# Kernel optimization log

Measured on AMD Instinct MI355X. Metric: run time of the kernel, lower is better.

Reference implementation:

```python
import jax, jax.numpy as jnp
import numpy as np

NUM_CLASSES = 80
FOCAL_ALPHA = 0.25
FOCAL_GAMMA = 2.0
HUBER_SIGMA = 3.0
REG_MEAN = 0.0
REG_STD = 0.2
IMG_H = 800.0
IMG_W = 800.0
B, A, M = 4, 100000, 32


def setup_inputs() -> dict:
    key = jax.random.key(0)
    k1, k2, k3, k4, k5, k6, k7 = jax.random.split(key, 7)
    classification = jax.random.uniform(k1, (B, A, NUM_CLASSES), dtype=jnp.float32)
    regression = jax.random.normal(k2, (B, A, 4), dtype=jnp.float32)
    # plausible anchors: centers inside image, sizes 16..256
    cx = jax.random.uniform(k3, (A,), minval=0.0, maxval=IMG_W)
    cy = jax.random.uniform(k4, (A,), minval=0.0, maxval=IMG_H)
    s = jax.random.uniform(k5, (A, 2), minval=16.0, maxval=256.0)
    anchors = jnp.stack([cx - s[:, 0] / 2, cy - s[:, 1] / 2,
                         cx + s[:, 0] / 2, cy + s[:, 1] / 2], axis=1).astype(jnp.float32)
    # annotations: [B, M, 5] = x1,y1,x2,y2,class
    xy = jax.random.uniform(k6, (B, M, 2), minval=0.0, maxval=650.0)
    wh = jax.random.uniform(k7, (B, M, 2), minval=30.0, maxval=150.0)
    cls = jax.random.randint(jax.random.fold_in(key, 9), (B, M, 1), 0, NUM_CLASSES).astype(jnp.float32)
    annotations = jnp.concatenate([xy, xy + wh, cls], axis=-1)
    return {"classification": classification, "regression": regression,
            "anchors": anchors, "annotations": annotations}


def _pairwise_iou(anchors, boxes):
    # anchors [A,4], boxes [M,4] -> [A,M]
    ix1 = jnp.maximum(anchors[:, None, 0], boxes[None, :, 0])
    iy1 = jnp.maximum(anchors[:, None, 1], boxes[None, :, 1])
    ix2 = jnp.minimum(anchors[:, None, 2], boxes[None, :, 2])
    iy2 = jnp.minimum(anchors[:, None, 3], boxes[None, :, 3])
    inter = jnp.clip(ix2 - ix1, 0.0) * jnp.clip(iy2 - iy1, 0.0)
    area_a = (anchors[:, 2] - anchors[:, 0]) * (anchors[:, 3] - anchors[:, 1])
    area_b = (boxes[:, 2] - boxes[:, 0]) * (boxes[:, 3] - boxes[:, 1])
    union = area_a[:, None] + area_b[None, :] - inter
    return inter / jnp.maximum(union, 1e-8)


def _targets(anchors, annotations):
    # per-image anchor assignment, vmapped over batch
    def per_image(ann):
        boxes = ann[:, :4]
        cls = ann[:, 4].astype(jnp.int32)
        ious = _pairwise_iou(anchors, boxes)          # [A,M]
        best = jnp.argmax(ious, axis=1)               # [A]
        best_iou = jnp.max(ious, axis=1)
        pos = best_iou >= 0.5
        ign = (best_iou > 0.4) & (~pos)
        states = jnp.where(pos, 1.0, jnp.where(ign, -1.0, 0.0))
        cx = (anchors[:, 0] + anchors[:, 2]) * 0.5
        cy = (anchors[:, 1] + anchors[:, 3]) * 0.5
        inside = (cx >= 0) & (cx < IMG_W) & (cy >= 0) & (cy < IMG_H)
        states = jnp.where(inside, states, -1.0)
        labels = jax.nn.one_hot(cls[best], NUM_CLASSES, dtype=jnp.float32) * pos[:, None]
        ab = boxes[best]                              # assigned gt boxes [A,4]
        aw = anchors[:, 2] - anchors[:, 0]
        ah = anchors[:, 3] - anchors[:, 1]
        t = jnp.stack([(ab[:, 0] - anchors[:, 0]) / aw,
                       (ab[:, 1] - anchors[:, 1]) / ah,
                       (ab[:, 2] - anchors[:, 2]) / aw,
                       (ab[:, 3] - anchors[:, 3]) / ah], axis=1)
        t = (t - REG_MEAN) / REG_STD
        return labels, t, states
    return jax.vmap(per_image)(annotations)


def reference(classification, regression, anchors, annotations):
    labels, reg_t, states = _targets(anchors, annotations)   # [B,A,K],[B,A,4],[B,A]
    num_pos = jnp.maximum(jnp.sum((states == 1.0).astype(jnp.float32)), 1.0)
    # focal loss over non-ignored anchors
    valid = (states != -1.0)[..., None].astype(jnp.float32)
    p = jnp.clip(classification, 1e-4, 1.0 - 1e-4)
    bce = -(labels * jnp.log(p) + (1.0 - labels) * jnp.log1p(-p))
    alpha_f = jnp.where(labels == 1.0, FOCAL_ALPHA, 1.0 - FOCAL_ALPHA)
    focal_w = alpha_f * jnp.where(labels == 1.0, 1.0 - p, p) ** FOCAL_GAMMA
    cls_loss = jnp.sum(focal_w * bce * valid) / num_pos
    # smooth L1 over positive anchors
    pos_m = (states == 1.0)[..., None].astype(jnp.float32)
    s2 = HUBER_SIGMA ** 2
    d = jnp.abs(regression - reg_t)
    l1 = jnp.where(d < 1.0 / s2, 0.5 * s2 * d * d, d - 0.5 / s2)
    reg_loss = jnp.sum(l1 * pos_m) / num_pos
    return cls_loss + reg_loss
```

## Files before the change

### kernel.cpp

```cpp
#include <hip/hip_runtime.h>

#define BB 4
#define AA 100000
#define MM 32
#define NC 80
#define GX 391
#define NBLK (GX * BB)


__device__ __forceinline__ void gld_lds16(const float4* g, float4* l) {
    __builtin_amdgcn_global_load_lds(
        (const __attribute__((address_space(1))) void*)g,
        (__attribute__((address_space(3))) void*)l,
        16, 0, 0);
}

#define FOCAL_K(vk, flatk)                                                  \
  {                                                                         \
    const int s    = (flatk) / 20;                                          \
    const int colb = ((flatk) - s * 20) * 4;                                \
    const int c    = scode[s];                                              \
    const float m  = (c != -2) ? 1.0f : 0.0f;                               \
    const float q0 = fminf(fmaxf((vk).x, 1e-4f), 0.9999f);                  \
    const float q1 = fminf(fmaxf((vk).y, 1e-4f), 0.9999f);                  \
    const float q2 = fminf(fmaxf((vk).z, 1e-4f), 0.9999f);                  \
    const float q3 = fminf(fmaxf((vk).w, 1e-4f), 0.9999f);                  \
    float sub = 0.0f;                                                       \
    sub += 0.75f * q0 * q0 * (-__logf(1.0f - q0));                          \
    sub += 0.75f * q1 * q1 * (-__logf(1.0f - q1));                          \
    sub += 0.75f * q2 * q2 * (-__logf(1.0f - q2));                          \
    sub += 0.75f * q3 * q3 * (-__logf(1.0f - q3));                          \
    csum += m * sub;                                                        \
    const unsigned rel = (unsigned)(c - colb);                              \
    if (rel < 4u) {      \
      const float p = (rel & 2u) ? ((rel & 1u) ? q3 : q2)                   \
                                 : ((rel & 1u) ? q1 : q0);                  \
      const float onem = 1.0f - p;                                          \
      csum += 0.25f * onem * onem * (-__logf(p))                            \
            - 0.75f * p * p * (-__logf(onem));                              \
    }                                                                       \
  }

#define FOCAL_BATCH(vv, batch)                                              \
  _Pragma("unroll")                                                         \
  for (int k = 0; k < 5; ++k) {                                             \
    const int flat = ((batch) * 5 + k) * 256 + tid;                         \
    FOCAL_K((vv)[k], flat)                                                  \
  }

__global__ __launch_bounds__(256) void fused_kernel(
    const float* __restrict__ anchors,
    const float* __restrict__ annotations,
    const float* __restrict__ regression,
    const float* __restrict__ cls,
    float* __restrict__ cls_part,
    float* __restrict__ reg_part,
    unsigned* __restrict__ pos_part)
{
    __shared__ float ann[MM * 5];
    __shared__ float areab[MM];
    __shared__ int scode[256];
    __shared__ float4 pre[5 * 256];
    const int b = blockIdx.y;
    const int tid = threadIdx.x;
    if (tid < MM * 5) ann[tid] = annotations[b * MM * 5 + tid];
    if (tid < MM) {
        const float bx1 = annotations[b * MM * 5 + tid * 5 + 0];
        const float by1 = annotations[b * MM * 5 + tid * 5 + 1];
        const float bx2 = annotations[b * MM * 5 + tid * 5 + 2];
        const float by2 = annotations[b * MM * 5 + tid * 5 + 3];
        areab[tid] = __fmul_rn(__fsub_rn(bx2, bx1), __fsub_rn(by2, by1));
    }
    __syncthreads();

    const int abase = blockIdx.x * 256;
    const int a = abase + tid;
    const float4* base4 = (const float4*)cls + ((size_t)b * AA + abase) * 20;
    const int maxflat = (abase + 256 <= AA) ? (5120 - 1) : ((AA - abase) * 20 - 1);

    float4 an = make_float4(0.f, 0.f, 0.f, 0.f);
    if (a < AA) an = ((const float4*)anchors)[a];

    #pragma unroll
    for (int k = 0; k < 5; ++k)
        gld_lds16(&base4[min(k * 256 + tid, maxflat)], &pre[k * 256 + tid]);

    float reg_sum = 0.0f;
    int pos_cnt = 0;
    int code = -2;

    if (a < AA) {
        const float ax1 = an.x, ay1 = an.y, ax2 = an.z, ay2 = an.w;
        const float area_a = __fmul_rn(__fsub_rn(ax2, ax1), __fsub_rn(ay2, ay1));

        float best_iou = -1.0f;
        int best = 0;
        #pragma unroll
        for (int j = 0; j < MM; ++j) {
            const float bx1 = ann[j * 5 + 0];
            const float by1 = ann[j * 5 + 1];
            const float bx2 = ann[j * 5 + 2];
            const float by2 = ann[j * 5 + 3];
            const float ix1 = fmaxf(ax1, bx1);
            const float iy1 = fmaxf(ay1, by1);
            const float ix2 = fminf(ax2, bx2);
            const float iy2 = fminf(ay2, by2);
            const float iw = fmaxf(__fsub_rn(ix2, ix1), 0.0f);
            const float ih = fmaxf(__fsub_rn(iy2, iy1), 0.0f);
            const float inter = __fmul_rn(iw, ih);
            const float uni = __fsub_rn(__fadd_rn(area_a, areab[j]), inter);
            const float iou = __fdiv_rn(inter, fmaxf(uni, 1e-8f));
            if (iou > best_iou) { best_iou = iou; best = j; }
        }

        const bool pos = best_iou >= 0.5f;
        const bool ign = (best_iou > 0.4f) && !pos;
        const float cx = (ax1 + ax2) * 0.5f;
        const float cy = (ay1 + ay2) * 0.5f;
        const bool inside = (cx >= 0.0f) && (cx < 800.0f) && (cy >= 0.0f) && (cy < 800.0f);

        const bool valid = inside && !ign;
        if (valid) code = pos ? (int)ann[best * 5 + 4] : -1;

        if (pos && inside) {
            pos_cnt = 1;
            const float aw = ax2 - ax1;
            const float ah = ay2 - ay1;
            const float bx1 = ann[best * 5 + 0];
            const float by1 = ann[best * 5 + 1];
            const float bx2 = ann[best * 5 + 2];
            const float by2 = ann[best * 5 + 3];
            float t[4];
            t[0] = ((bx1 - ax1) / aw) / 0.2f;
            t[1] = ((by1 - ay1) / ah) / 0.2f;
            t[2] = ((bx2 - ax2) / aw) / 0.2f;
            t[3] = ((by2 - ay2) / ah) / 0.2f;
            const float* rg = regression + (((size_t)b * AA + a) * 4);
            #pragma unroll
            for (int k = 0; k < 4; ++k) {
                const float d = fabsf(rg[k] - t[k]);
                reg_sum += (d < (1.0f / 9.0f)) ? (4.5f * d * d) : (d - (0.5f / 9.0f));
            }
        }
    }
    scode[tid] = code;
    __syncthreads();

    float csum = 0.0f;

    float4 v1[5];
    #pragma unroll
    for (int k = 0; k < 5; ++k) v1[k] = base4[min((5 + k) * 256 + tid, maxflat)];

    float4 v0[5];
    #pragma unroll
    for (int k = 0; k < 5; ++k) v0[k] = pre[k * 256 + tid];
    FOCAL_BATCH(v0, 0)

    float4 v2[5];
    #pragma unroll
    for (int k = 0; k < 5; ++k) v2[k] = base4[min((10 + k) * 256 + tid, maxflat)];
    FOCAL_BATCH(v1, 1)

    float4 v3[5];
    #pragma unroll
    for (int k = 0; k < 5; ++k) v3[k] = base4[min((15 + k) * 256 + tid, maxflat)];
    FOCAL_BATCH(v2, 2)
    FOCAL_BATCH(v3, 3)

    #pragma unroll
    for (int off = 32; off > 0; off >>= 1) {
        csum    += __shfl_down(csum, off);
        reg_sum += __shfl_down(reg_sum, off);
        pos_cnt += __shfl_down(pos_cnt, off);
    }
    __shared__ float wc[4], wr[4];
    __shared__ int   wp[4];
    const int wave = tid >> 6, lane = tid & 63;
    if (lane == 0) { wc[wave] = csum; wr[wave] = reg_sum; wp[wave] = pos_cnt; }
    __syncthreads();
    if (tid == 0) {
        const int idx = b * GX + blockIdx.x;
        cls_part[idx] = wc[0] + wc[1] + wc[2] + wc[3];
        reg_part[idx] = wr[0] + wr[1] + wr[2] + wr[3];
        pos_part[idx] = (unsigned)(wp[0] + wp[1] + wp[2] + wp[3]);
    }
}

__global__ __launch_bounds__(256) void finalize_kernel(
    const float* __restrict__ cls_part,
    const float* __restrict__ reg_part,
    const unsigned* __restrict__ pos_part,
    float* __restrict__ out)
{
    float cs = 0.0f, rs = 0.0f;
    unsigned pc = 0;
    for (int i = threadIdx.x; i < NBLK; i += 256) {
        cs += cls_part[i];
        rs += reg_part[i];
        pc += pos_part[i];
    }
    #pragma unroll
    for (int off = 32; off > 0; off >>= 1) {
        cs += __shfl_down(cs, off);
        rs += __shfl_down(rs, off);
        pc += __shfl_down(pc, off);
    }
    __shared__ float wc[4], wr[4];
    __shared__ unsigned wp[4];
    const int wave = threadIdx.x >> 6, lane = threadIdx.x & 63;
    if (lane == 0) { wc[wave] = cs; wr[wave] = rs; wp[wave] = pc; }
    __syncthreads();
    if (threadIdx.x == 0) {
        const float csum = wc[0] + wc[1] + wc[2] + wc[3];
        const float rsum = wr[0] + wr[1] + wr[2] + wr[3];
        const float np = fmaxf((float)(wp[0] + wp[1] + wp[2] + wp[3]), 1.0f);
        out[0] = (csum + rsum) / np;
    }
}

extern "C" void kernel_launch(void* const* d_in, const int* in_sizes, int n_in,
                              void* d_out, int out_size, void* d_ws, size_t ws_size,
                              hipStream_t stream)
{
    const float* classification = (const float*)d_in[0];
    const float* regression     = (const float*)d_in[1];
    const float* anchors        = (const float*)d_in[2];
    const float* annotations    = (const float*)d_in[3];
    float* out = (float*)d_out;

    float*    cls_part = (float*)d_ws;
    float*    reg_part = cls_part + NBLK;
    unsigned* pos_part = (unsigned*)(reg_part + NBLK);

    dim3 grid(GX, BB);
    fused_kernel<<<grid, 256, 0, stream>>>(anchors, annotations, regression,
                                           classification, cls_part, reg_part, pos_part);
    finalize_kernel<<<1, 256, 0, stream>>>(cls_part, reg_part, pos_part, out);
}
```

Baseline: 196.8 us.

## Fuse finalize into main kernel via last-block ticket and prefetch earlier

```diff
diff --git a/kernel.cpp b/kernel.cpp
--- a/kernel.cpp
+++ b/kernel.cpp
@@ -55,12 +55,15 @@
     const float* __restrict__ cls,
     float* __restrict__ cls_part,
     float* __restrict__ reg_part,
-    unsigned* __restrict__ pos_part)
+    unsigned* __restrict__ pos_part,
+    unsigned* __restrict__ ticket,
+    float* __restrict__ out)
 {
     __shared__ float ann[MM * 5];
     __shared__ float areab[MM];
     __shared__ int scode[256];
     __shared__ float4 pre[5 * 256];
+    __shared__ bool amLast;
     const int b = blockIdx.y;
     const int tid = threadIdx.x;
     if (tid < MM * 5) ann[tid] = annotations[b * MM * 5 + tid];
@@ -143,28 +146,29 @@
             }
         }
     }
+
+    float4 v1[5];
+    #pragma unroll
+    for (int k = 0; k < 5; ++k) v1[k] = base4[min((5 + k) * 256 + tid, maxflat)];
+
     scode[tid] = code;
     __syncthreads();
 
     float csum = 0.0f;
 
-    float4 v1[5];
-    #pragma unroll
-    for (int k = 0; k < 5; ++k) v1[k] = base4[min((5 + k) * 256 + tid, maxflat)];
+    float4 v2[5];
+    #pragma unroll
+    for (int k = 0; k < 5; ++k) v2[k] = base4[min((10 + k) * 256 + tid, maxflat)];
 
     float4 v0[5];
     #pragma unroll
     for (int k = 0; k < 5; ++k) v0[k] = pre[k * 256 + tid];
     FOCAL_BATCH(v0, 0)
 
-    float4 v2[5];
-    #pragma unroll
-    for (int k = 0; k < 5; ++k) v2[k] = base4[min((10 + k) * 256 + tid, maxflat)];
+    float4 v3[5];
+    #pragma unroll
+    for (int k = 0; k < 5; ++k) v3[k] = base4[min((15 + k) * 256 + tid, maxflat)];
     FOCAL_BATCH(v1, 1)
-
-    float4 v3[5];
-    #pragma unroll
-    for (int k = 0; k < 5; ++k) v3[k] = base4[min((15 + k) * 256 + tid, maxflat)];
     FOCAL_BATCH(v2, 2)
     FOCAL_BATCH(v3, 3)
 
@@ -184,18 +188,18 @@
         cls_part[idx] = wc[0] + wc[1] + wc[2] + wc[3];
         reg_part[idx] = wr[0] + wr[1] + wr[2] + wr[3];
         pos_part[idx] = (unsigned)(wp[0] + wp[1] + wp[2] + wp[3]);
-    }
-}
-
-__global__ __launch_bounds__(256) void finalize_kernel(
-    const float* __restrict__ cls_part,
-    const float* __restrict__ reg_part,
-    const unsigned* __restrict__ pos_part,
-    float* __restrict__ out)
-{
+        __threadfence();
+        const unsigned t = __hip_atomic_fetch_add(ticket, 1u, __ATOMIC_ACQ_REL,
+                                                  __HIP_MEMORY_SCOPE_AGENT);
+        amLast = (t == (unsigned)(NBLK - 1));
+    }
+    __syncthreads();
+    if (!amLast) return;
+
+    __threadfence();
     float cs = 0.0f, rs = 0.0f;
     unsigned pc = 0;
-    for (int i = threadIdx.x; i < NBLK; i += 256) {
+    for (int i = tid; i < NBLK; i += 256) {
         cs += cls_part[i];
         rs += reg_part[i];
         pc += pos_part[i];
@@ -206,16 +210,15 @@
         rs += __shfl_down(rs, off);
         pc += __shfl_down(pc, off);
     }
-    __shared__ float wc[4], wr[4];
-    __shared__ unsigned wp[4];
-    const int wave = threadIdx.x >> 6, lane = threadIdx.x & 63;
-    if (lane == 0) { wc[wave] = cs; wr[wave] = rs; wp[wave] = pc; }
-    __syncthreads();
-    if (threadIdx.x == 0) {
-        const float csum = wc[0] + wc[1] + wc[2] + wc[3];
-        const float rsum = wr[0] + wr[1] + wr[2] + wr[3];
-        const float np = fmaxf((float)(wp[0] + wp[1] + wp[2] + wp[3]), 1.0f);
-        out[0] = (csum + rsum) / np;
+    __shared__ float fc[4], fr[4];
+    __shared__ unsigned fp[4];
+    if (lane == 0) { fc[wave] = cs; fr[wave] = rs; fp[wave] = pc; }
+    __syncthreads();
+    if (tid == 0) {
+        const float csumf = fc[0] + fc[1] + fc[2] + fc[3];
+        const float rsumf = fr[0] + fr[1] + fr[2] + fr[3];
+        const float np = fmaxf((float)(fp[0] + fp[1] + fp[2] + fp[3]), 1.0f);
+        out[0] = (csumf + rsumf) / np;
     }
 }
 
@@ -232,9 +235,12 @@
     float*    cls_part = (float*)d_ws;
     float*    reg_part = cls_part + NBLK;
     unsigned* pos_part = (unsigned*)(reg_part + NBLK);
+    unsigned* ticket   = pos_part + NBLK;
+
+    hipMemsetAsync(ticket, 0, sizeof(unsigned), stream);
 
     dim3 grid(GX, BB);
     fused_kernel<<<grid, 256, 0, stream>>>(anchors, annotations, regression,
-                                           classification, cls_part, reg_part, pos_part);
-    finalize_kernel<<<1, 256, 0, stream>>>(cls_part, reg_part, pos_part, out);
+                                           classification, cls_part, reg_part,
+                                           pos_part, ticket, out);
 }
```

Measured after the change: 319.9 us. 62.5% more time.
